# Performance work log

Measured on AMD Instinct MI355X. Metric: run time of the kernel, lower is better.

The kernel has to match this reference:

```python
import jax, jax.numpy as jnp
import numpy as np

D_MODEL = 1024
N_HEADS = 16
D_K = D_MODEL // N_HEADS


def setup_inputs() -> dict:
    key = jax.random.key(0)
    ks = jax.random.split(key, 12)
    B, S, D = 4, 2048, D_MODEL
    scale = 1.0 / np.sqrt(D)
    inp = {
        'query': jax.random.normal(ks[0], (B, S, D), jnp.float32),
        'key': jax.random.normal(ks[1], (B, S, D), jnp.float32),
        'value': jax.random.normal(ks[2], (B, S, D), jnp.float32),
        'Wq': jax.random.normal(ks[3], (D, D), jnp.float32) * scale,
        'bq': jax.random.normal(ks[4], (D,), jnp.float32) * 0.02,
        'Wk': jax.random.normal(ks[5], (D, D), jnp.float32) * scale,
        'bk': jax.random.normal(ks[6], (D,), jnp.float32) * 0.02,
        'Wv': jax.random.normal(ks[7], (D, D), jnp.float32) * scale,
        'bv': jax.random.normal(ks[8], (D,), jnp.float32) * 0.02,
        'Wo': jax.random.normal(ks[9], (D, D), jnp.float32) * scale,
        'bo': jax.random.normal(ks[10], (D,), jnp.float32) * 0.02,
    }
    return inp


def reference(query, key, value, Wq, bq, Wk, bk, Wv, bv, Wo, bo):
    B, S, D = query.shape
    # torch nn.Linear: y = x @ W^T + b
    def proj(x, W, b):
        y = jnp.einsum('bsd,ed->bse', x, W) + b
        # [B,S,D] -> [B,H,S,d_k]
        return y.reshape(B, S, N_HEADS, D_K).transpose(0, 2, 1, 3)

    q = proj(query, Wq, bq)
    k = proj(key, Wk, bk)
    v = proj(value, Wv, bv)

    scores = jnp.einsum('bhqd,bhkd->bhqk', q, k) / jnp.sqrt(jnp.float32(D_K))
    attn = jax.nn.softmax(scores, axis=-1)  # dropout = identity (eval mode)
    out = jnp.einsum('bhqk,bhkd->bhqd', attn, v)
    out = out.transpose(0, 2, 1, 3).reshape(B, S, D)
    return jnp.einsum('bsd,ed->bse', out, Wo) + bo
```

## Files before the change

### kernel.cpp

```cpp
#include <hip/hip_runtime.h>
#include <hip/hip_bf16.h>
#include <cstdint>
#include <cstddef>


#define BATCH   4
#define SEQ     2048
#define D_MODEL 1024
#define NHEADS  16
#define DK      64

typedef __attribute__((ext_vector_type(8))) __bf16 bf16x8_t;
typedef __attribute__((ext_vector_type(4))) float  f32x4;

__device__ inline unsigned int pack2(float lo, float hi) {
  __hip_bfloat162 h = __float22bfloat162_rn(make_float2(lo, hi));
  union { __hip_bfloat162 h; unsigned int u; } c; c.h = h; return c.u;
}
__device__ inline unsigned short f2bf(float f) { return (unsigned short)pack2(f, f); }

#if __has_builtin(__builtin_amdgcn_exp2f)
__device__ inline float fexp2(float x) { return __builtin_amdgcn_exp2f(x); }
#else
__device__ inline float fexp2(float x) { return __expf(x * 0.6931471805599453f); }
#endif

__device__ inline void cvt8(const float* __restrict__ s, unsigned short* __restrict__ d) {
  const float4 a = *(const float4*)s;
  const float4 b = *(const float4*)(s + 4);
  uint4 r;
  r.x = pack2(a.x, a.y); r.y = pack2(a.z, a.w);
  r.z = pack2(b.x, b.y); r.w = pack2(b.z, b.w);
  *(uint4*)d = r;
}

typedef __attribute__((address_space(3))) unsigned int lds_u32_t;
typedef const __attribute__((address_space(1))) unsigned int glb_u32_t;
__device__ inline void gld16(const unsigned short* g, unsigned short* l) {
  __builtin_amdgcn_global_load_lds((glb_u32_t*)(uintptr_t)g,
                                   (lds_u32_t*)(unsigned int)(uintptr_t)l, 16, 0, 0);
}

__global__ __launch_bounds__(256) void cvt3_kernel(
    const float* __restrict__ a, const float* __restrict__ b, const float* __restrict__ c,
    unsigned short* __restrict__ oa, unsigned short* __restrict__ ob, unsigned short* __restrict__ oc)
{
  const float* s = (blockIdx.y == 0) ? a : (blockIdx.y == 1) ? b : c;
  unsigned short* d = (blockIdx.y == 0) ? oa : (blockIdx.y == 1) ? ob : oc;
  const size_t i = ((size_t)blockIdx.x * 256 + threadIdx.x) * 8;
  cvt8(s + i, d + i);
}
__global__ __launch_bounds__(256) void cvt4_kernel(
    const float* __restrict__ a, const float* __restrict__ b,
    const float* __restrict__ c, const float* __restrict__ dd,
    unsigned short* __restrict__ oa, unsigned short* __restrict__ ob,
    unsigned short* __restrict__ oc, unsigned short* __restrict__ od)
{
  const float* s = (blockIdx.y == 0) ? a : (blockIdx.y == 1) ? b : (blockIdx.y == 2) ? c : dd;
  unsigned short* d = (blockIdx.y == 0) ? oa : (blockIdx.y == 1) ? ob : (blockIdx.y == 2) ? oc : od;
  const size_t i = ((size_t)blockIdx.x * 256 + threadIdx.x) * 8;
  cvt8(s + i, d + i);
}

__device__ inline void gemm_core(const unsigned short* __restrict__ A,
                                 const unsigned short* __restrict__ W,
                                 unsigned short* a_lds, unsigned short* b_lds,
                                 int m0, int n0, f32x4 (&acc)[4][4])
{
  const int tid  = threadIdx.x;
  const int lane = tid & 63;
  const int wv   = tid >> 6;
  const int l15  = lane & 15;
  const int quad = lane >> 4;
  const int wm = (wv & 1) * 64;
  const int wn = (wv >> 1) * 64;

  const int srow = tid >> 2;
  const int sch  = (tid & 3) ^ (srow & 3);
  const unsigned short* Ap0 = A + (size_t)(m0 + srow) * D_MODEL + sch * 8;
  const unsigned short* Ap1 = Ap0 + (size_t)64 * D_MODEL;
  const unsigned short* Wp0 = W + (size_t)(n0 + srow) * D_MODEL + sch * 8;
  const unsigned short* Wp1 = Wp0 + (size_t)64 * D_MODEL;
  unsigned short* al0 = a_lds + wv * 512;
  unsigned short* al1 = a_lds + 2048 + wv * 512;
  unsigned short* bl0 = b_lds + wv * 512;
  unsigned short* bl1 = b_lds + 2048 + wv * 512;

  const int pq = (quad ^ (l15 & 3)) * 8;

  for (int k0 = 0; k0 < D_MODEL; k0 += 32) {
    __syncthreads();
    gld16(Ap0 + k0, al0);
    gld16(Ap1 + k0, al1);
    gld16(Wp0 + k0, bl0);
    gld16(Wp1 + k0, bl1);
    __syncthreads();

    bf16x8_t af[4], bfr[4];
#pragma unroll
    for (int i = 0; i < 4; ++i)
      af[i] = *(const bf16x8_t*)&a_lds[(wm + i * 16 + l15) * 32 + pq];
#pragma unroll
    for (int j = 0; j < 4; ++j)
      bfr[j] = *(const bf16x8_t*)&b_lds[(wn + j * 16 + l15) * 32 + pq];

#pragma unroll
    for (int i = 0; i < 4; ++i)
#pragma unroll
      for (int j = 0; j < 4; ++j)
        acc[i][j] = __builtin_amdgcn_mfma_f32_16x16x32_bf16(af[i], bfr[j], acc[i][j], 0, 0, 0);
  }
}

__global__ __launch_bounds__(256) void qkv_kernel(
    const unsigned short* __restrict__ qb, const unsigned short* __restrict__ kb,
    const unsigned short* __restrict__ vb,
    const unsigned short* __restrict__ wq, const unsigned short* __restrict__ wk,
    const unsigned short* __restrict__ wvp,
    const float* __restrict__ bq, const float* __restrict__ bk, const float* __restrict__ bv,
    unsigned short* __restrict__ Qws, unsigned short* __restrict__ Kws,
    unsigned short* __restrict__ Vws)
{
  __shared__ unsigned short a_lds[128 * 32];
  __shared__ unsigned short b_lds[128 * 32];

  const int z = blockIdx.z;
  const unsigned short* A = (z == 0) ? qb : (z == 1) ? kb : vb;
  const unsigned short* W = (z == 0) ? wq : (z == 1) ? wk : wvp;
  const float* bias       = (z == 0) ? bq : (z == 1) ? bk : bv;
  unsigned short* C       = (z == 0) ? Qws : (z == 1) ? Kws : Vws;
  const int m0 = blockIdx.x * 128;
  const int n0 = blockIdx.y * 128;

  f32x4 acc[4][4];
#pragma unroll
  for (int i = 0; i < 4; ++i)
#pragma unroll
    for (int j = 0; j < 4; ++j)
      acc[i][j] = (f32x4){0.f, 0.f, 0.f, 0.f};

  gemm_core(A, W, a_lds, b_lds, m0, n0, acc);

  const int tid  = threadIdx.x;
  const int lane = tid & 63;
  const int wv   = tid >> 6;
  const int l15  = lane & 15;
  const int quad = lane >> 4;
  const int wm = (wv & 1) * 64;
  const int wn = (wv >> 1) * 64;
  if (z == 2) {
    for (int j = 0; j < 4; ++j) {
      const int n = n0 + wn + j * 16 + l15;
      const int hh = n >> 6, dd = n & 63;
      const float bvl = bias[n];
      for (int i = 0; i < 4; ++i) {
        const int mbase = m0 + wm + i * 16 + quad * 4;
        const int bb = mbase >> 11, ss = mbase & 2047;
        uint2 w2 = make_uint2(pack2(acc[i][j][0] + bvl, acc[i][j][1] + bvl),
                              pack2(acc[i][j][2] + bvl, acc[i][j][3] + bvl));
        *(uint2*)(C + (((size_t)bb * NHEADS + hh) * DK + dd) * SEQ + ss) = w2;
      }
    }
  } else {
    const float oscale = (z == 0) ? 0.18033688011112042f : 1.0f;
    for (int j = 0; j < 4; ++j) {
      const int n = n0 + wn + j * 16 + l15;
      const int hh = n >> 6, dd = n & 63;
      const float bvl = bias[n];
      for (int i = 0; i < 4; ++i) {
        const int mbase = m0 + wm + i * 16 + quad * 4;
        const int bb = mbase >> 11, ss = mbase & 2047;
        unsigned short* dst = C + (((size_t)bb * NHEADS + hh) * SEQ + ss) * DK + dd;
        for (int r = 0; r < 4; ++r)
          dst[(size_t)r * DK] = f2bf((acc[i][j][r] + bvl) * oscale);
      }
    }
  }
}

__global__ __launch_bounds__(256) void outproj_kernel(
    const unsigned short* __restrict__ A, const unsigned short* __restrict__ W,
    const float* __restrict__ bias, float* __restrict__ C)
{
  __shared__ unsigned short a_lds[128 * 32];
  __shared__ unsigned short b_lds[128 * 32];
  const int m0 = blockIdx.x * 128;
  const int n0 = blockIdx.y * 128;

  f32x4 acc[4][4];
#pragma unroll
  for (int i = 0; i < 4; ++i)
#pragma unroll
    for (int j = 0; j < 4; ++j)
      acc[i][j] = (f32x4){0.f, 0.f, 0.f, 0.f};

  gemm_core(A, W, a_lds, b_lds, m0, n0, acc);

  const int tid  = threadIdx.x;
  const int lane = tid & 63;
  const int wv   = tid >> 6;
  const int l15  = lane & 15;
  const int quad = lane >> 4;
  const int wm = (wv & 1) * 64;
  const int wn = (wv >> 1) * 64;
  for (int j = 0; j < 4; ++j) {
    const int n = n0 + wn + j * 16 + l15;
    const float bvl = bias[n];
    for (int i = 0; i < 4; ++i) {
      const int mbase = m0 + wm + i * 16 + quad * 4;
      for (int r = 0; r < 4; ++r)
        C[(size_t)(mbase + r) * D_MODEL + n] = acc[i][j][r] + bvl;
    }
  }
}

__global__ __launch_bounds__(256) void attn_kernel(
    const unsigned short* __restrict__ Q,
    const unsigned short* __restrict__ K,
    const unsigned short* __restrict__ Vt,
    unsigned short* __restrict__ Oattn)
{
  __shared__ unsigned short k_sw[2 * 64 * 64];
  __shared__ unsigned short vt_sw[2 * 64 * 64];
  __shared__ unsigned short pt_sw[4 * 16 * 64];

  const int tid  = threadIdx.x;
  const int lane = tid & 63;
  const int wv   = tid >> 6;
  const int l15  = lane & 15;
  const int quad = lane >> 4;
  const int bh   = blockIdx.x;
  const int q0   = blockIdx.y * 64;
  const size_t hoff = (size_t)bh * SEQ * DK;
  const unsigned short* Qh  = Q  + hoff;
  const unsigned short* Kh  = K  + hoff;
  const unsigned short* Vth = Vt + hoff;

  bf16x8_t qf0, qf1;
  {
    const unsigned short* qr = Qh + (size_t)(q0 + wv * 16 + l15) * DK;
    qf0 = *(const bf16x8_t*)(qr + quad * 8);
    qf1 = *(const bf16x8_t*)(qr + 32 + quad * 8);
  }

  f32x4 o[4];
#pragma unroll
  for (int t = 0; t < 4; ++t) o[t] = (f32x4){0.f, 0.f, 0.f, 0.f};
  float mval = -1e30f, lval = 0.f;

  const int sr = lane >> 3;
  const int pc = lane & 7;
  const int r0 = wv * 16 + sr;
  const int r1 = r0 + 8;
  const int sem0 = pc ^ (r0 & 7) ^ (r0 >> 3);
  const int sem1 = pc ^ (r1 & 7) ^ (r1 >> 3);
  const unsigned short* KsA = Kh  + (size_t)r0 * DK  + sem0 * 8;
  const unsigned short* KsB = Kh  + (size_t)r1 * DK  + sem1 * 8;
  const unsigned short* VsA = Vth + (size_t)r0 * SEQ + sem0 * 8;
  const unsigned short* VsB = Vth + (size_t)r1 * SEQ + sem1 * 8;
  unsigned short* kd = k_sw  + wv * 1024;
  unsigned short* vd = vt_sw + wv * 1024;

#define STAGE(buf, key0) do {                                        \
    gld16(KsA + (size_t)(key0) * DK, kd + (buf) * 4096);             \
    gld16(KsB + (size_t)(key0) * DK, kd + (buf) * 4096 + 512);       \
    gld16(VsA + (key0),              vd + (buf) * 4096);             \
    gld16(VsB + (key0),              vd + (buf) * 4096 + 512);       \
  } while (0)

  const int swz_l15 = (l15 & 7) ^ (l15 >> 3);
  unsigned short* pt_base = pt_sw + wv * 1024;

  STAGE(0, 0);
  __syncthreads();

  int cur = 0;
  for (int kb = 0; kb < SEQ / 64; ++kb) {
    if (kb + 1 < SEQ / 64) STAGE(cur ^ 1, (kb + 1) * 64);

    const unsigned short* kcur = k_sw  + cur * 4096;
    const unsigned short* vcur = vt_sw + cur * 4096;

    f32x4 s[4];
    __builtin_amdgcn_s_setprio(1);
#pragma unroll
    for (int t = 0; t < 4; ++t) {
      const int row = t * 16 + l15;
      const int sw  = (row & 7) ^ (row >> 3);
      bf16x8_t kf0 = *(const bf16x8_t*)&kcur[row * 64 + ((quad ^ sw) << 3)];
      bf16x8_t kf1 = *(const bf16x8_t*)&kcur[row * 64 + (((quad | 4) ^ sw) << 3)];
      f32x4 z = (f32x4){0.f, 0.f, 0.f, 0.f};
      z = __builtin_amdgcn_mfma_f32_16x16x32_bf16(kf0, qf0, z, 0, 0, 0);
      z = __builtin_amdgcn_mfma_f32_16x16x32_bf16(kf1, qf1, z, 0, 0, 0);
      s[t] = z;
    }
    __builtin_amdgcn_s_setprio(0);

    float mx = s[0][0];
#pragma unroll
    for (int t = 0; t < 4; ++t)
#pragma unroll
      for (int r = 0; r < 4; ++r) mx = fmaxf(mx, s[t][r]);
    mx = fmaxf(mx, __shfl_xor(mx, 16));
    mx = fmaxf(mx, __shfl_xor(mx, 32));
    if (__any(mx > mval + 8.0f)) {
      const float mnew  = fmaxf(mval, mx);
      const float alpha = fexp2(mval - mnew);
      mval = mnew;
      lval *= alpha;
#pragma unroll
      for (int t = 0; t < 4; ++t) o[t] *= alpha;
    }
    float rs = 0.f;
    float p[4][4];
#pragma unroll
    for (int t = 0; t < 4; ++t)
#pragma unroll
      for (int r = 0; r < 4; ++r) { p[t][r] = fexp2(s[t][r] - mval); rs += p[t][r]; }
    rs += __shfl_xor(rs, 16);
    rs += __shfl_xor(rs, 32);
    lval += rs;

#pragma unroll
    for (int t = 0; t < 4; ++t) {
      const int chunk = 2 * t + (quad >> 1);
      unsigned short* dst = pt_base + l15 * 64 + ((chunk ^ swz_l15) << 3) + (quad & 1) * 4;
      *(uint2*)dst = make_uint2(pack2(p[t][0], p[t][1]), pack2(p[t][2], p[t][3]));
    }
    asm volatile("s_waitcnt lgkmcnt(0)" ::: "memory");

    bf16x8_t pf0 = *(const bf16x8_t*)(pt_base + l15 * 64 + ((quad ^ swz_l15) << 3));
    bf16x8_t pf1 = *(const bf16x8_t*)(pt_base + l15 * 64 + (((quad | 4) ^ swz_l15) << 3));

    __builtin_amdgcn_s_setprio(1);
#pragma unroll
    for (int nt = 0; nt < 4; ++nt) {
      const int row = nt * 16 + l15;
      const int sw  = (row & 7) ^ (row >> 3);
      bf16x8_t vf0 = *(const bf16x8_t*)&vcur[row * 64 + ((quad ^ sw) << 3)];
      bf16x8_t vf1 = *(const bf16x8_t*)&vcur[row * 64 + (((quad | 4) ^ sw) << 3)];
      o[nt] = __builtin_amdgcn_mfma_f32_16x16x32_bf16(vf0, pf0, o[nt], 0, 0, 0);
      o[nt] = __builtin_amdgcn_mfma_f32_16x16x32_bf16(vf1, pf1, o[nt], 0, 0, 0);
    }
    __builtin_amdgcn_s_setprio(0);

    __syncthreads();
    cur ^= 1;
  }
#undef STAGE

  const int bb = bh >> 4, hh = bh & 15;
  const float inv = 1.0f / lval;
  unsigned short* orow = Oattn + (size_t)(bb * SEQ + q0 + wv * 16 + l15) * D_MODEL + hh * DK + quad * 4;
#pragma unroll
  for (int nt = 0; nt < 4; ++nt) {
    f32x4 v = o[nt];
    *(uint2*)(orow + nt * 16) = make_uint2(pack2(v[0] * inv, v[1] * inv),
                                           pack2(v[2] * inv, v[3] * inv));
  }
}

extern "C" void kernel_launch(void* const* d_in, const int* in_sizes, int n_in,
                              void* d_out, int out_size, void* d_ws, size_t ws_size,
                              hipStream_t stream) {
  const float* query = (const float*)d_in[0];
  const float* key   = (const float*)d_in[1];
  const float* value = (const float*)d_in[2];
  const float* Wq    = (const float*)d_in[3];
  const float* bq    = (const float*)d_in[4];
  const float* Wk    = (const float*)d_in[5];
  const float* bk    = (const float*)d_in[6];
  const float* Wv    = (const float*)d_in[7];
  const float* bv    = (const float*)d_in[8];
  const float* Wo    = (const float*)d_in[9];
  const float* bo    = (const float*)d_in[10];

  const size_t E  = (size_t)BATCH * SEQ * D_MODEL;
  const size_t WE = (size_t)D_MODEL * D_MODEL;
  unsigned short* ws  = (unsigned short*)d_ws;
  unsigned short* Qws = ws;
  unsigned short* Kws = ws + E;
  unsigned short* Vws = ws + 2 * E;
  unsigned short* qb  = ws + 3 * E;
  unsigned short* kb  = ws + 4 * E;
  unsigned short* vb  = ws + 5 * E;
  unsigned short* wqb = ws + 6 * E;
  unsigned short* wkb = wqb + WE;
  unsigned short* wvb = wqb + 2 * WE;
  unsigned short* wob = wqb + 3 * WE;
  unsigned short* Aws = qb;

  cvt3_kernel<<<dim3(E / 2048, 3), 256, 0, stream>>>(query, key, value, qb, kb, vb);
  cvt4_kernel<<<dim3(WE / 2048, 4), 256, 0, stream>>>(Wq, Wk, Wv, Wo, wqb, wkb, wvb, wob);

  qkv_kernel<<<dim3(BATCH * SEQ / 128, D_MODEL / 128, 3), 256, 0, stream>>>(
      qb, kb, vb, wqb, wkb, wvb, bq, bk, bv, Qws, Kws, Vws);
  attn_kernel<<<dim3(BATCH * NHEADS, SEQ / 64), 256, 0, stream>>>(Qws, Kws, Vws, Aws);
  outproj_kernel<<<dim3(BATCH * SEQ / 128, D_MODEL / 128), 256, 0, stream>>>(
      Aws, wob, bo, (float*)d_out);
}
```

Measured before the change: 399.5 us.

## Use 8-wave attention blocks sharing K/V tiles and pass P via shuffles

The attention kernel now runs 512 threads (8 waves) per block over 128 query rows, so each staged K/V tile is shared by twice as many waves and each thread issues half as many global-to-LDS copies. The P matrix is rearranged into the MFMA B-operand layout with cross-lane shuffles instead of a round trip through shared memory, which removes the P scratch buffer and its LDS wait. Launch bounds ask for 6 waves per SIMD, which limits registers per thread. The extra shuffle and select instructions replace the LDS traffic and could cost ALU time.

```diff
diff --git a/kernel.cpp b/kernel.cpp
--- a/kernel.cpp
+++ b/kernel.cpp
@@ -214,7 +214,7 @@
   }
 }
 
-__global__ __launch_bounds__(256) void attn_kernel(
+__global__ __launch_bounds__(512, 6) void attn_kernel(
     const unsigned short* __restrict__ Q,
     const unsigned short* __restrict__ K,
     const unsigned short* __restrict__ Vt,
@@ -222,7 +222,6 @@
 {
   __shared__ unsigned short k_sw[2 * 64 * 64];
   __shared__ unsigned short vt_sw[2 * 64 * 64];
-  __shared__ unsigned short pt_sw[4 * 16 * 64];
 
   const int tid  = threadIdx.x;
   const int lane = tid & 63;
@@ -230,7 +229,7 @@
   const int l15  = lane & 15;
   const int quad = lane >> 4;
   const int bh   = blockIdx.x;
-  const int q0   = blockIdx.y * 64;
+  const int q0   = blockIdx.y * 128;
   const size_t hoff = (size_t)bh * SEQ * DK;
   const unsigned short* Qh  = Q  + hoff;
   const unsigned short* Kh  = K  + hoff;
@@ -248,28 +247,23 @@
   for (int t = 0; t < 4; ++t) o[t] = (f32x4){0.f, 0.f, 0.f, 0.f};
   float mval = -1e30f, lval = 0.f;
 
-  const int sr = lane >> 3;
-  const int pc = lane & 7;
-  const int r0 = wv * 16 + sr;
-  const int r1 = r0 + 8;
-  const int sem0 = pc ^ (r0 & 7) ^ (r0 >> 3);
-  const int sem1 = pc ^ (r1 & 7) ^ (r1 >> 3);
-  const unsigned short* KsA = Kh  + (size_t)r0 * DK  + sem0 * 8;
-  const unsigned short* KsB = Kh  + (size_t)r1 * DK  + sem1 * 8;
-  const unsigned short* VsA = Vth + (size_t)r0 * SEQ + sem0 * 8;
-  const unsigned short* VsB = Vth + (size_t)r1 * SEQ + sem1 * 8;
-  unsigned short* kd = k_sw  + wv * 1024;
-  unsigned short* vd = vt_sw + wv * 1024;
+  const int sr  = lane >> 3;
+  const int pc  = lane & 7;
+  const int row = wv * 8 + sr;
+  const int sem = pc ^ sr ^ wv;
+  const unsigned short* KsA = Kh  + (size_t)row * DK  + sem * 8;
+  const unsigned short* VsA = Vth + (size_t)row * SEQ + sem * 8;
+  unsigned short* kd = k_sw  + wv * 512;
+  unsigned short* vd = vt_sw + wv * 512;
 
 #define STAGE(buf, key0) do {                                        \
     gld16(KsA + (size_t)(key0) * DK, kd + (buf) * 4096);             \
-    gld16(KsB + (size_t)(key0) * DK, kd + (buf) * 4096 + 512);       \
     gld16(VsA + (key0),              vd + (buf) * 4096);             \
-    gld16(VsB + (key0),              vd + (buf) * 4096 + 512);       \
   } while (0)
 
-  const int swz_l15 = (l15 & 7) ^ (l15 >> 3);
-  unsigned short* pt_base = pt_sw + wv * 1024;
+  const int srcA = l15 + ((quad & 1) << 5);
+  const int srcB = srcA + 16;
+  const int hi   = quad >> 1;
 
   STAGE(0, 0);
   __syncthreads();
@@ -285,10 +279,10 @@
     __builtin_amdgcn_s_setprio(1);
 #pragma unroll
     for (int t = 0; t < 4; ++t) {
-      const int row = t * 16 + l15;
-      const int sw  = (row & 7) ^ (row >> 3);
-      bf16x8_t kf0 = *(const bf16x8_t*)&kcur[row * 64 + ((quad ^ sw) << 3)];
-      bf16x8_t kf1 = *(const bf16x8_t*)&kcur[row * 64 + (((quad | 4) ^ sw) << 3)];
+      const int r = t * 16 + l15;
+      const int sw = (r & 7) ^ (r >> 3);
+      bf16x8_t kf0 = *(const bf16x8_t*)&kcur[r * 64 + ((quad ^ sw) << 3)];
+      bf16x8_t kf1 = *(const bf16x8_t*)&kcur[r * 64 + (((quad | 4) ^ sw) << 3)];
       f32x4 z = (f32x4){0.f, 0.f, 0.f, 0.f};
       z = __builtin_amdgcn_mfma_f32_16x16x32_bf16(kf0, qf0, z, 0, 0, 0);
       z = __builtin_amdgcn_mfma_f32_16x16x32_bf16(kf1, qf1, z, 0, 0, 0);
@@ -312,33 +306,51 @@
       for (int t = 0; t < 4; ++t) o[t] *= alpha;
     }
     float rs = 0.f;
-    float p[4][4];
-#pragma unroll
-    for (int t = 0; t < 4; ++t)
-#pragma unroll
-      for (int r = 0; r < 4; ++r) { p[t][r] = fexp2(s[t][r] - mval); rs += p[t][r]; }
+    unsigned int u[4][2];
+#pragma unroll
+    for (int t = 0; t < 4; ++t) {
+      const float p0 = fexp2(s[t][0] - mval);
+      const float p1 = fexp2(s[t][1] - mval);
+      const float p2 = fexp2(s[t][2] - mval);
+      const float p3 = fexp2(s[t][3] - mval);
+      rs += (p0 + p1) + (p2 + p3);
+      u[t][0] = pack2(p0, p1);
+      u[t][1] = pack2(p2, p3);
+    }
     rs += __shfl_xor(rs, 16);
     rs += __shfl_xor(rs, 32);
     lval += rs;
 
-#pragma unroll
-    for (int t = 0; t < 4; ++t) {
-      const int chunk = 2 * t + (quad >> 1);
-      unsigned short* dst = pt_base + l15 * 64 + ((chunk ^ swz_l15) << 3) + (quad & 1) * 4;
-      *(uint2*)dst = make_uint2(pack2(p[t][0], p[t][1]), pack2(p[t][2], p[t][3]));
-    }
-    asm volatile("s_waitcnt lgkmcnt(0)" ::: "memory");
-
-    bf16x8_t pf0 = *(const bf16x8_t*)(pt_base + l15 * 64 + ((quad ^ swz_l15) << 3));
-    bf16x8_t pf1 = *(const bf16x8_t*)(pt_base + l15 * 64 + (((quad | 4) ^ swz_l15) << 3));
+    unsigned int w0[4], w1[4];
+#pragma unroll
+    for (int c = 0; c < 2; ++c) {
+      unsigned int* wc = c ? w1 : w0;
+      const unsigned int uA0 = u[2 * c][0],     uA1 = u[2 * c][1];
+      const unsigned int uB0 = u[2 * c + 1][0], uB1 = u[2 * c + 1][1];
+      unsigned int a, b;
+      a = (unsigned int)__shfl((int)uA0, srcA); b = (unsigned int)__shfl((int)uB0, srcA);
+      wc[0] = hi ? b : a;
+      a = (unsigned int)__shfl((int)uA1, srcA); b = (unsigned int)__shfl((int)uB1, srcA);
+      wc[1] = hi ? b : a;
+      a = (unsigned int)__shfl((int)uA0, srcB); b = (unsigned int)__shfl((int)uB0, srcB);
+      wc[2] = hi ? b : a;
+      a = (unsigned int)__shfl((int)uA1, srcB); b = (unsigned int)__shfl((int)uB1, srcB);
+      wc[3] = hi ? b : a;
+    }
+    union Cv { unsigned int w[4]; bf16x8_t v; };
+    Cv cv0, cv1;
+    cv0.w[0] = w0[0]; cv0.w[1] = w0[1]; cv0.w[2] = w0[2]; cv0.w[3] = w0[3];
+    cv1.w[0] = w1[0]; cv1.w[1] = w1[1]; cv1.w[2] = w1[2]; cv1.w[3] = w1[3];
+    const bf16x8_t pf0 = cv0.v;
+    const bf16x8_t pf1 = cv1.v;
 
     __builtin_amdgcn_s_setprio(1);
 #pragma unroll
     for (int nt = 0; nt < 4; ++nt) {
-      const int row = nt * 16 + l15;
-      const int sw  = (row & 7) ^ (row >> 3);
-      bf16x8_t vf0 = *(const bf16x8_t*)&vcur[row * 64 + ((quad ^ sw) << 3)];
-      bf16x8_t vf1 = *(const bf16x8_t*)&vcur[row * 64 + (((quad | 4) ^ sw) << 3)];
+      const int r = nt * 16 + l15;
+      const int sw = (r & 7) ^ (r >> 3);
+      bf16x8_t vf0 = *(const bf16x8_t*)&vcur[r * 64 + ((quad ^ sw) << 3)];
+      bf16x8_t vf1 = *(const bf16x8_t*)&vcur[r * 64 + (((quad | 4) ^ sw) << 3)];
       o[nt] = __builtin_amdgcn_mfma_f32_16x16x32_bf16(vf0, pf0, o[nt], 0, 0, 0);
       o[nt] = __builtin_amdgcn_mfma_f32_16x16x32_bf16(vf1, pf1, o[nt], 0, 0, 0);
     }
@@ -395,7 +407,7 @@
 
   qkv_kernel<<<dim3(BATCH * SEQ / 128, D_MODEL / 128, 3), 256, 0, stream>>>(
       qb, kb, vb, wqb, wkb, wvb, bq, bk, bv, Qws, Kws, Vws);
-  attn_kernel<<<dim3(BATCH * NHEADS, SEQ / 64), 256, 0, stream>>>(Qws, Kws, Vws, Aws);
+  attn_kernel<<<dim3(BATCH * NHEADS, SEQ / 128), 512, 0, stream>>>(Qws, Kws, Vws, Aws);
   outproj_kernel<<<dim3(BATCH * SEQ / 128, D_MODEL / 128), 256, 0, stream>>>(
       Aws, wob, bo, (float*)d_out);
 }
```

Result: no change. 402.5 us (+0.7%).
